# Performance work log

Measured on AMD Instinct MI355X. Metric: run time of the kernel, lower is better.

The kernel has to match this reference:

```python
import jax, jax.numpy as jnp
import numpy as np

B, NS, D, NE = 4096, 64, 256, 16  # walkers, determinant slots, d_model, electrons


def setup_inputs() -> dict:
    key = jax.random.key(0)
    k_y, k_up, k_dn, k_r = jax.random.split(key, 4)
    y = jax.random.normal(k_y, (B, NS, D), dtype=jnp.float32)
    # xavier_uniform over (d_model, Ne) fan axes
    limit = np.sqrt(6.0 / (D + NE)).astype(np.float32)
    M1_up_real = jax.random.uniform(k_up, (NS, D, NE), dtype=jnp.float32, minval=-limit, maxval=limit)
    M1_down_real = jax.random.uniform(k_dn, (NS, D, NE), dtype=jnp.float32, minval=-limit, maxval=limit)
    # R: Ne distinct orbital-row indices per walker in [0, 2*Ns)
    keys = jax.random.split(k_r, B)
    R = jax.vmap(lambda k: jax.random.permutation(k, 2 * NS)[:NE])(keys).astype(jnp.int32)
    return {"y": y, "M1_up_real": M1_up_real, "M1_down_real": M1_down_real, "R": R}


def reference(y, M1_up_real, M1_down_real, R):
    # orbitals: per-slot linear map of features -> Ne orbital values
    orb_up = jnp.einsum('bnd,nde->bne', y, M1_up_real)      # (B, Ns, Ne)
    orb_dn = jnp.einsum('bnd,nde->bne', y, M1_down_real)    # (B, Ns, Ne)
    orbitals = jnp.concatenate((orb_up, orb_dn), axis=1)     # (B, 2*Ns, Ne)
    # gather Ne rows per walker -> batched square matrices (B, Ne, Ne)
    A = jnp.take_along_axis(orbitals, R[:, :, None], axis=1)
    sign, logabsdet = jnp.linalg.slogdet(A)
    cdtype = jnp.complex64
    amp = logabsdet.astype(cdtype) + jnp.log(sign.astype(cdtype))
    return jnp.where(jnp.isnan(amp), -jnp.inf, amp)          # (B,) complex64
```

## Files before the change

### kernel.cpp

```cpp
#include <hip/hip_runtime.h>
#include <math.h>

#define BWALK 4096
#define NS 64
#define DD 256
#define NE 16
#define NSLOT 128
#define CHUNK 1024

typedef __attribute__((ext_vector_type(4))) float f32x4;
typedef __attribute__((ext_vector_type(8))) short s16x8;

union Frag { s16x8 v; unsigned u[4]; };

__device__ inline unsigned rne_bf16(float x) {
    unsigned u = __float_as_uint(x);
    return (u + 0x7fffu + ((u >> 16) & 1u)) >> 16;
}
__device__ inline float bf16_to_f(unsigned h) { return __uint_as_float(h << 16); }

__global__ __launch_bounds__(256) void orbitals_kernel(
    const float* __restrict__ y,
    const float* __restrict__ Mup,
    const float* __restrict__ Mdn,
    const int* __restrict__ R,
    float* __restrict__ A)
{
    const int n   = blockIdx.y;
    const int b0  = blockIdx.x * CHUNK;
    const int tid = threadIdx.x;
    const int lane = tid & 63;
    const int wv   = tid >> 6;

    __shared__ float sM[DD * NE];
    __shared__ int   sCode[CHUNK];
    __shared__ int   wsum[4];

    int m[4];
    int cnt = 0;
    #pragma unroll
    for (int q = 0; q < 4; ++q) {
        const int b = b0 + tid * 4 + q;
        const int4* rp = (const int4*)(R + (size_t)b * NE);
        int mi = -1;
        #pragma unroll
        for (int t4 = 0; t4 < 4; ++t4) {
            const int4 r4 = rp[t4];
            if (r4.x == n) mi = t4 * 4 + 0;
            if (r4.y == n) mi = t4 * 4 + 1;
            if (r4.z == n) mi = t4 * 4 + 2;
            if (r4.w == n) mi = t4 * 4 + 3;
        }
        m[q] = mi;
        cnt += (mi >= 0) ? 1 : 0;
    }

    int incl = cnt;
    #pragma unroll
    for (int off = 1; off < 64; off <<= 1) {
        const int x = __shfl_up(incl, off, 64);
        if (lane >= off) incl += x;
    }
    if (lane == 63) wsum[wv] = incl;
    __syncthreads();
    int base = incl - cnt;
    #pragma unroll
    for (int w = 0; w < 3; ++w) if (w < wv) base += wsum[w];
    const int total = wsum[0] + wsum[1] + wsum[2] + wsum[3];

    {
        int p = base;
        #pragma unroll
        for (int q = 0; q < 4; ++q) {
            if (m[q] >= 0) {
                const int b = b0 + tid * 4 + q;
                sCode[p++] = (b << 4) | m[q];
            }
        }
    }

    {
        const float* Msrc = (n < NS ? Mup : Mdn) + (size_t)(n & (NS - 1)) * (DD * NE);
        const f32x4* src = (const f32x4*)Msrc;
        f32x4* dst = (f32x4*)sM;
        #pragma unroll
        for (int p = 0; p < 4; ++p) dst[p * 256 + tid] = src[p * 256 + tid];
    }
    __syncthreads();

    if (total == 0) return;

    const int e  = lane & 15;
    const int kg = lane >> 4;

    Frag bhi[8], blo[8];
    #pragma unroll
    for (int kc = 0; kc < 8; ++kc) {
        #pragma unroll
        for (int t = 0; t < 4; ++t) {
            const int k0 = kc * 32 + kg * 8 + 2 * t;
            const float f0 = sM[k0 * 16 + e];
            const float f1 = sM[(k0 + 1) * 16 + e];
            const unsigned h0 = rne_bf16(f0), h1 = rne_bf16(f1);
            bhi[kc].u[t] = h0 | (h1 << 16);
            const unsigned l0 = rne_bf16(f0 - bf16_to_f(h0));
            const unsigned l1 = rne_bf16(f1 - bf16_to_f(h1));
            blo[kc].u[t] = l0 | (l1 << 16);
        }
    }

    const int slot = n & (NS - 1);

    for (int g = wv * 16; g < total; g += 64) {
        const int me = g + e;
        const int code = sCode[me < total ? me : (total - 1)];
        const int b = code >> 4;
        const float* yrow = y + ((size_t)b * NS + slot) * DD + kg * 8;

        f32x4 v[8][2];
        #pragma unroll
        for (int kc = 0; kc < 8; ++kc) {
            const f32x4* p = (const f32x4*)(yrow + kc * 32);
            v[kc][0] = p[0];
            v[kc][1] = p[1];
        }

        f32x4 acc = {0.f, 0.f, 0.f, 0.f};
        #pragma unroll
        for (int kc = 0; kc < 8; ++kc) {
            Frag ahi, alo;
            #pragma unroll
            for (int t = 0; t < 4; ++t) {
                const float f0 = v[kc][t >> 1][(t & 1) * 2];
                const float f1 = v[kc][t >> 1][(t & 1) * 2 + 1];
                const unsigned h0 = rne_bf16(f0), h1 = rne_bf16(f1);
                ahi.u[t] = h0 | (h1 << 16);
                const unsigned l0 = rne_bf16(f0 - bf16_to_f(h0));
                const unsigned l1 = rne_bf16(f1 - bf16_to_f(h1));
                alo.u[t] = l0 | (l1 << 16);
            }
            acc = __builtin_amdgcn_mfma_f32_16x16x32_bf16(ahi.v, bhi[kc].v, acc, 0, 0, 0);
            acc = __builtin_amdgcn_mfma_f32_16x16x32_bf16(ahi.v, blo[kc].v, acc, 0, 0, 0);
            acc = __builtin_amdgcn_mfma_f32_16x16x32_bf16(alo.v, bhi[kc].v, acc, 0, 0, 0);
        }

        #pragma unroll
        for (int r = 0; r < 4; ++r) {
            const int j = kg * 4 + r;
            const int jcode = __shfl(code, j, 16);
            if (g + j < total) A[(size_t)jcode * NE + e] = acc[r];
        }
    }
}

__global__ __launch_bounds__(256) void lu_det_kernel(
    const float* __restrict__ A, float* __restrict__ out, int mode)
{
    const int tid = threadIdx.x;
    const int w = blockIdx.x * 16 + (tid >> 4);
    const int lane = tid & 15;

    float a[NE];
    {
        const f32x4* p = (const f32x4*)(A + ((size_t)w * NE + lane) * NE);
        #pragma unroll
        for (int q = 0; q < 4; ++q) {
            const f32x4 vv = p[q];
            a[q * 4 + 0] = vv[0]; a[q * 4 + 1] = vv[1];
            a[q * 4 + 2] = vv[2]; a[q * 4 + 3] = vv[3];
        }
    }

    unsigned used = 0u;
    float logabs = 0.0f;
    int neg = 0;
    int perm[NE];

    #pragma unroll
    for (int k = 0; k < NE; ++k) {
        float v = ((used >> lane) & 1u) ? -1.0f : fabsf(a[k]);
        int bi = lane;
        #pragma unroll
        for (int off = 8; off > 0; off >>= 1) {
            const float ov = __shfl_xor(v, off, 16);
            const int   oi = __shfl_xor(bi, off, 16);
            if (ov > v || (ov == v && oi < bi)) { v = ov; bi = oi; }
        }
        const int p = bi;
        perm[k] = p;
        const float pivval = __shfl(a[k], p, 16);
        const bool active = (((used >> lane) & 1u) == 0u) && (lane != p);
        const float mlt = active ? (a[k] / pivval) : 0.0f;
        #pragma unroll
        for (int ee = k + 1; ee < NE; ++ee) {
            const float pe = __shfl(a[ee], p, 16);
            a[ee] = fmaf(-mlt, pe, a[ee]);
        }
        used |= (1u << p);
        logabs += logf(fabsf(pivval));
        neg ^= (pivval < 0.0f) ? 1 : 0;
    }

    int inv = 0;
    #pragma unroll
    for (int k1 = 0; k1 < NE; ++k1) {
        #pragma unroll
        for (int k2 = k1 + 1; k2 < NE; ++k2)
            inv ^= (perm[k1] > perm[k2]) ? 1 : 0;
    }
    neg ^= inv;

    if (lane == 0) {
        float re = logabs;
        float im = neg ? 3.14159274101257324f : 0.0f;
        if (__builtin_isnan(re)) { re = -INFINITY; im = 0.0f; }
        else if (re == -INFINITY) { im = 0.0f; }
        if (mode == 0) { out[2 * w] = re; out[2 * w + 1] = im; }
        else           { out[w] = re; }
    }
}

__global__ __launch_bounds__(256) void outputheaddet_kernel(
    const float* __restrict__ y,
    const float* __restrict__ Mup,
    const float* __restrict__ Mdn,
    const int* __restrict__ R,
    float* __restrict__ out,
    int mode)
{
    const int b = blockIdx.x;
    const int tid = threadIdx.x;

    __shared__ int   sR[NE];
    __shared__ float sY[NE][DD];
    __shared__ float sA[NE][NE + 1];

    if (tid < NE) sR[tid] = R[b * NE + tid];
    __syncthreads();

    {
        const int i  = tid >> 4;
        const int d0 = (tid & 15) * 16;
        const int n    = sR[i];
        const int slot = n & (NS - 1);
        const float4* yp = reinterpret_cast<const float4*>(
            y + (((size_t)b * NS + slot) * DD + d0));
        float4 v0 = yp[0], v1 = yp[1], v2 = yp[2], v3 = yp[3];
        float4* dst = reinterpret_cast<float4*>(&sY[i][d0]);
        dst[0] = v0; dst[1] = v1; dst[2] = v2; dst[3] = v3;
    }
    __syncthreads();

    {
        const int i = tid >> 4;
        const int e = tid & 15;
        const int n    = sR[i];
        const int slot = n & (NS - 1);
        const float* Mp = (n < NS ? Mup : Mdn) + (size_t)slot * (DD * NE) + e;
        float acc = 0.0f;
        #pragma unroll 8
        for (int d = 0; d < DD; ++d)
            acc = fmaf(sY[i][d], Mp[(size_t)d * NE], acc);
        sA[i][e] = acc;
    }
    __syncthreads();

    if (tid >= NE) return;

    const int lane = tid;
    float a[NE];
    #pragma unroll
    for (int e = 0; e < NE; ++e) a[e] = sA[lane][e];

    unsigned used = 0u;
    float logabs = 0.0f;
    int neg = 0;
    int perm[NE];

    #pragma unroll
    for (int k = 0; k < NE; ++k) {
        float v = ((used >> lane) & 1u) ? -1.0f : fabsf(a[k]);
        int bi = lane;
        #pragma unroll
        for (int off = 8; off > 0; off >>= 1) {
            float ov = __shfl_xor(v, off, 16);
            int   oi = __shfl_xor(bi, off, 16);
            if (ov > v || (ov == v && oi < bi)) { v = ov; bi = oi; }
        }
        const int p = bi;
        perm[k] = p;
        const float pivval = __shfl(a[k], p, 16);
        const bool active = (((used >> lane) & 1u) == 0u) && (lane != p);
        const float mlt = active ? (a[k] / pivval) : 0.0f;
        #pragma unroll
        for (int e = k + 1; e < NE; ++e) {
            const float pe = __shfl(a[e], p, 16);
            a[e] = fmaf(-mlt, pe, a[e]);
        }
        used |= (1u << p);
        logabs += logf(fabsf(pivval));
        neg ^= (pivval < 0.0f) ? 1 : 0;
    }

    int inv = 0;
    #pragma unroll
    for (int k1 = 0; k1 < NE; ++k1) {
        #pragma unroll
        for (int k2 = k1 + 1; k2 < NE; ++k2)
            inv ^= (perm[k1] > perm[k2]) ? 1 : 0;
    }
    neg ^= inv;

    if (lane == 0) {
        float re = logabs;
        float im = neg ? 3.14159274101257324f : 0.0f;
        if (__builtin_isnan(re)) { re = -INFINITY; im = 0.0f; }
        else if (re == -INFINITY) { im = 0.0f; }
        if (mode == 0) { out[2 * b] = re; out[2 * b + 1] = im; }
        else           { out[b] = re; }
    }
}

extern "C" void kernel_launch(void* const* d_in, const int* in_sizes, int n_in,
                              void* d_out, int out_size, void* d_ws, size_t ws_size,
                              hipStream_t stream) {
    const float* y   = (const float*)d_in[0];
    const float* Mup = (const float*)d_in[1];
    const float* Mdn = (const float*)d_in[2];
    const int*   R   = (const int*)d_in[3];
    float* out = (float*)d_out;

    const int mode = (out_size >= 2 * BWALK) ? 0 : 1;
    const size_t needA = (size_t)BWALK * NE * NE * sizeof(float);

    if (ws_size >= needA) {
        float* A = (float*)d_ws;
        hipLaunchKernelGGL(orbitals_kernel, dim3(BWALK / CHUNK, NSLOT), dim3(256), 0, stream,
                           y, Mup, Mdn, R, A);
        hipLaunchKernelGGL(lu_det_kernel, dim3(BWALK / 16), dim3(256), 0, stream,
                           A, out, mode);
    } else {
        hipLaunchKernelGGL(outputheaddet_kernel, dim3(BWALK), dim3(256), 0, stream,
                           y, Mup, Mdn, R, out, mode);
    }
}
```

Measured before the change: 42.88 us.

## Precompute bf16 hi/lo weight fragments in a separate kernel and halve chunk size

Adds a pre-pass kernel that converts the M weights once into MFMA-ready bf16 hi/lo fragments in the workspace. The orbitals kernel now loads these fragments straight from global memory instead of staging fp32 M in shared memory and splitting it in every block. CHUNK drops from 1024 to 512, doubling the block count, and the three MFMA chains use separate accumulators so they can run without waiting on each other. In exchange it adds a kernel launch, needs a larger workspace, and reloads the fragments on every loop iteration.

Result: slower. 43.79 us (+2.1%).

```diff
diff --git a/kernel.cpp b/kernel.cpp
--- a/kernel.cpp
+++ b/kernel.cpp
@@ -6,12 +6,12 @@
 #define DD 256
 #define NE 16
 #define NSLOT 128
-#define CHUNK 1024
+#define CHUNK 512
 
 typedef __attribute__((ext_vector_type(4))) float f32x4;
 typedef __attribute__((ext_vector_type(8))) short s16x8;
 
-union Frag { s16x8 v; unsigned u[4]; };
+union Frag  { s16x8 v; unsigned u[4]; uint4 q; };
 
 __device__ inline unsigned rne_bf16(float x) {
     unsigned u = __float_as_uint(x);
@@ -19,11 +19,44 @@
 }
 __device__ inline float bf16_to_f(unsigned h) { return __uint_as_float(h << 16); }
 
+__global__ __launch_bounds__(256) void convert_m_kernel(
+    const float* __restrict__ Mup,
+    const float* __restrict__ Mdn,
+    uint4* __restrict__ Mhi,
+    uint4* __restrict__ Mlo)
+{
+    const int t = blockIdx.x * 256 + threadIdx.x;
+    const int n    = t >> 9;
+    const int kc   = (t >> 6) & 7;
+    const int lane = t & 63;
+    const int kg = lane >> 4;
+    const int e  = lane & 15;
+
+    const float* Msrc = (n < NS ? Mup : Mdn) + (size_t)(n & (NS - 1)) * (DD * NE);
+
+    unsigned h[8], l[8];
+    #pragma unroll
+    for (int j = 0; j < 8; ++j) {
+        const int k = kc * 32 + kg * 8 + j;
+        const float f = Msrc[k * 16 + e];
+        const unsigned hh = rne_bf16(f);
+        h[j] = hh;
+        l[j] = rne_bf16(f - bf16_to_f(hh));
+    }
+    uint4 vh, vl;
+    vh.x = h[0] | (h[1] << 16); vh.y = h[2] | (h[3] << 16);
+    vh.z = h[4] | (h[5] << 16); vh.w = h[6] | (h[7] << 16);
+    vl.x = l[0] | (l[1] << 16); vl.y = l[2] | (l[3] << 16);
+    vl.z = l[4] | (l[5] << 16); vl.w = l[6] | (l[7] << 16);
+    Mhi[t] = vh;
+    Mlo[t] = vl;
+}
+
 __global__ __launch_bounds__(256) void orbitals_kernel(
     const float* __restrict__ y,
-    const float* __restrict__ Mup,
-    const float* __restrict__ Mdn,
     const int* __restrict__ R,
+    const uint4* __restrict__ Mhi,
+    const uint4* __restrict__ Mlo,
     float* __restrict__ A)
 {
     const int n   = blockIdx.y;
@@ -32,15 +65,14 @@
     const int lane = tid & 63;
     const int wv   = tid >> 6;
 
-    __shared__ float sM[DD * NE];
-    __shared__ int   sCode[CHUNK];
-    __shared__ int   wsum[4];
-
-    int m[4];
+    __shared__ int sCode[CHUNK];
+    __shared__ int wsum[4];
+
+    int m[2];
     int cnt = 0;
     #pragma unroll
-    for (int q = 0; q < 4; ++q) {
-        const int b = b0 + tid * 4 + q;
+    for (int q = 0; q < 2; ++q) {
+        const int b = b0 + tid * 2 + q;
         const int4* rp = (const int4*)(R + (size_t)b * NE);
         int mi = -1;
         #pragma unroll
@@ -67,49 +99,25 @@
     #pragma unroll
     for (int w = 0; w < 3; ++w) if (w < wv) base += wsum[w];
     const int total = wsum[0] + wsum[1] + wsum[2] + wsum[3];
-
     {
         int p = base;
         #pragma unroll
-        for (int q = 0; q < 4; ++q) {
+        for (int q = 0; q < 2; ++q) {
             if (m[q] >= 0) {
-                const int b = b0 + tid * 4 + q;
+                const int b = b0 + tid * 2 + q;
                 sCode[p++] = (b << 4) | m[q];
             }
         }
     }
-
-    {
-        const float* Msrc = (n < NS ? Mup : Mdn) + (size_t)(n & (NS - 1)) * (DD * NE);
-        const f32x4* src = (const f32x4*)Msrc;
-        f32x4* dst = (f32x4*)sM;
-        #pragma unroll
-        for (int p = 0; p < 4; ++p) dst[p * 256 + tid] = src[p * 256 + tid];
-    }
     __syncthreads();
 
     if (total == 0) return;
 
     const int e  = lane & 15;
     const int kg = lane >> 4;
-
-    Frag bhi[8], blo[8];
-    #pragma unroll
-    for (int kc = 0; kc < 8; ++kc) {
-        #pragma unroll
-        for (int t = 0; t < 4; ++t) {
-            const int k0 = kc * 32 + kg * 8 + 2 * t;
-            const float f0 = sM[k0 * 16 + e];
-            const float f1 = sM[(k0 + 1) * 16 + e];
-            const unsigned h0 = rne_bf16(f0), h1 = rne_bf16(f1);
-            bhi[kc].u[t] = h0 | (h1 << 16);
-            const unsigned l0 = rne_bf16(f0 - bf16_to_f(h0));
-            const unsigned l1 = rne_bf16(f1 - bf16_to_f(h1));
-            blo[kc].u[t] = l0 | (l1 << 16);
-        }
-    }
-
     const int slot = n & (NS - 1);
+    const uint4* bhp = Mhi + ((size_t)n * 8) * 64 + lane;
+    const uint4* blp = Mlo + ((size_t)n * 8) * 64 + lane;
 
     for (int g = wv * 16; g < total; g += 64) {
         const int me = g + e;
@@ -124,8 +132,16 @@
             v[kc][0] = p[0];
             v[kc][1] = p[1];
         }
-
-        f32x4 acc = {0.f, 0.f, 0.f, 0.f};
+        Frag BH[8], BL[8];
+        #pragma unroll
+        for (int kc = 0; kc < 8; ++kc) {
+            BH[kc].q = bhp[kc * 64];
+            BL[kc].q = blp[kc * 64];
+        }
+
+        f32x4 acc0 = {0.f, 0.f, 0.f, 0.f};
+        f32x4 acc1 = {0.f, 0.f, 0.f, 0.f};
+        f32x4 acc2 = {0.f, 0.f, 0.f, 0.f};
         #pragma unroll
         for (int kc = 0; kc < 8; ++kc) {
             Frag ahi, alo;
@@ -139,10 +155,11 @@
                 const unsigned l1 = rne_bf16(f1 - bf16_to_f(h1));
                 alo.u[t] = l0 | (l1 << 16);
             }
-            acc = __builtin_amdgcn_mfma_f32_16x16x32_bf16(ahi.v, bhi[kc].v, acc, 0, 0, 0);
-            acc = __builtin_amdgcn_mfma_f32_16x16x32_bf16(ahi.v, blo[kc].v, acc, 0, 0, 0);
-            acc = __builtin_amdgcn_mfma_f32_16x16x32_bf16(alo.v, bhi[kc].v, acc, 0, 0, 0);
-        }
+            acc0 = __builtin_amdgcn_mfma_f32_16x16x32_bf16(ahi.v, BH[kc].v, acc0, 0, 0, 0);
+            acc1 = __builtin_amdgcn_mfma_f32_16x16x32_bf16(ahi.v, BL[kc].v, acc1, 0, 0, 0);
+            acc2 = __builtin_amdgcn_mfma_f32_16x16x32_bf16(alo.v, BH[kc].v, acc2, 0, 0, 0);
+        }
+        const f32x4 acc = acc0 + (acc1 + acc2);
 
         #pragma unroll
         for (int r = 0; r < 4; ++r) {
@@ -331,12 +348,21 @@
     float* out = (float*)d_out;
 
     const int mode = (out_size >= 2 * BWALK) ? 0 : 1;
-    const size_t needA = (size_t)BWALK * NE * NE * sizeof(float);
-
-    if (ws_size >= needA) {
-        float* A = (float*)d_ws;
+
+    const size_t frag_bytes = (size_t)NSLOT * 8 * 64 * 16;
+    const size_t off_Mlo = frag_bytes;
+    const size_t off_A   = 2 * frag_bytes;
+    const size_t need    = off_A + (size_t)BWALK * NE * NE * sizeof(float);
+
+    if (ws_size >= need) {
+        uint4* Mhi = (uint4*)d_ws;
+        uint4* Mlo = (uint4*)((char*)d_ws + off_Mlo);
+        float* A   = (float*)((char*)d_ws + off_A);
+
+        hipLaunchKernelGGL(convert_m_kernel, dim3(NSLOT * 8 * 64 / 256), dim3(256), 0, stream,
+                           Mup, Mdn, Mhi, Mlo);
         hipLaunchKernelGGL(orbitals_kernel, dim3(BWALK / CHUNK, NSLOT), dim3(256), 0, stream,
-                           y, Mup, Mdn, R, A);
+                           y, R, Mhi, Mlo, A);
         hipLaunchKernelGGL(lu_det_kernel, dim3(BWALK / 16), dim3(256), 0, stream,
                            A, out, mode);
     } else {
```
